# Kernel tuning notes

Measured on AMD Instinct MI355X. Metric: run time of the kernel, lower is better.

The kernel has to match this reference:

```python
import jax, jax.numpy as jnp
import numpy as np

N = 50000
E = 800000
IN_C, HID, LAT = 256, 128, 64


def setup_inputs() -> dict:
    key = jax.random.key(0)
    ks = jax.random.split(key, 8)
    x = jax.random.normal(ks[0], (N, IN_C), dtype=jnp.float32)
    edge_index = jax.random.randint(ks[1], (2, E), 0, N, dtype=jnp.int64)
    # Glorot-ish scaled weights (PyG GCNConv: Linear weight + separate bias)
    W1 = jax.random.normal(ks[2], (IN_C, HID), dtype=jnp.float32) / np.sqrt(IN_C)
    b1 = jnp.zeros((HID,), dtype=jnp.float32)
    Wmu = jax.random.normal(ks[3], (HID, LAT), dtype=jnp.float32) / np.sqrt(HID)
    bmu = jnp.zeros((LAT,), dtype=jnp.float32)
    Wlv = jax.random.normal(ks[4], (HID, LAT), dtype=jnp.float32) / np.sqrt(HID)
    blv = jnp.zeros((LAT,), dtype=jnp.float32)
    return {"x": x, "edge_index": edge_index, "W1": W1, "b1": b1,
            "Wmu": Wmu, "bmu": bmu, "Wlv": Wlv, "blv": blv}


def gcn_conv(x, edge_index, W, b):
    """PyG GCNConv: add self-loops, sym-normalize, transform, scatter-add."""
    n = x.shape[0]
    loop = jnp.arange(n, dtype=edge_index.dtype)
    row = jnp.concatenate([edge_index[0], loop])  # source
    col = jnp.concatenate([edge_index[1], loop])  # target
    deg = jax.ops.segment_sum(jnp.ones_like(col, dtype=x.dtype), col, num_segments=n)
    dinv = jax.lax.rsqrt(jnp.maximum(deg, 1e-12))  # deg >= 1 due to self-loops
    norm = dinv[row] * dinv[col]                   # [E+N]
    h = x @ W                                      # transform first (smaller width)
    msg = h[row] * norm[:, None]                   # [E+N, out] gathered messages
    out = jax.ops.segment_sum(msg, col, num_segments=n)
    return out + b


def reference(x, edge_index, W1, b1, Wmu, bmu, Wlv, blv):
    h = jax.nn.relu(gcn_conv(x, edge_index, W1, b1))
    # dropout p=0.0 -> identity
    mu = gcn_conv(h, edge_index, Wmu, bmu)
    logvar = gcn_conv(h, edge_index, Wlv, blv)
    return (mu, logvar)
```

## Files before the change

kernel.cpp:

```cpp
#include <hip/hip_runtime.h>
#include <stdint.h>

#define NN   50000
#define NE   800000
#define INC  256
#define HID  128
#define LAT  64

typedef unsigned short u16;
typedef short v8s __attribute__((ext_vector_type(8)));
typedef float v4f __attribute__((ext_vector_type(4)));

#define SLAB_OFF 0
#define OFFS_OFF 802816
#define W1P_OFF  881216
#define W2P_OFF  897600
#define G1_OFF   905792

#define NBIN        196
#define OFFS_STRIDE 200
#define NSLAB       784

#define G2_OFFU  8388608
#define C2_CNT   8388608
#define C2_DINV  8438608
#define C2_BKT   8488608

#define GB    782

__device__ __forceinline__ u16 f2b(float f) {
    union { float f; uint32_t i; } c; c.f = f;
    uint32_t r = c.i + 0x7FFF + ((c.i >> 16) & 1);
    return (u16)(r >> 16);
}
__device__ __forceinline__ float blo(unsigned u) { return __uint_as_float(u << 16); }
__device__ __forceinline__ float bhi(unsigned u) { return __uint_as_float(u & 0xffff0000u); }

__device__ void pack1_body(const float* __restrict__ W1, u16* __restrict__ W1P, int b) {
    int tg = b * 256 + threadIdx.x;
    int ks = tg >> 9, rem = tg & 511;
    int nt = rem >> 6, lane = rem & 63;
    int quad = lane >> 4, l15 = lane & 15;
    u16 o[8];
    #pragma unroll
    for (int j = 0; j < 8; j++)
        o[j] = f2b(W1[(long)(ks * 32 + quad * 8 + j) * HID + nt * 16 + l15]);
    *(ushort4*)(W1P + (long)tg * 8)     = make_ushort4(o[0], o[1], o[2], o[3]);
    *(ushort4*)(W1P + (long)tg * 8 + 4) = make_ushort4(o[4], o[5], o[6], o[7]);
}

__device__ void pack2_body(const float* __restrict__ Wmu, const float* __restrict__ Wlv,
                           u16* __restrict__ W2P, int b) {
    int tg = b * 256 + threadIdx.x;
    int ks = tg >> 9, rem = tg & 511;
    int nt = rem >> 6, lane = rem & 63;
    int quad = lane >> 4, l15 = lane & 15;
    const float* W = (nt < 4) ? Wmu : Wlv;
    int ntl = (nt < 4) ? nt : nt - 4;
    u16 o[8];
    #pragma unroll
    for (int j = 0; j < 8; j++)
        o[j] = f2b(W[(long)(ks * 32 + quad * 8 + j) * LAT + ntl * 16 + l15]);
    *(ushort4*)(W2P + (long)tg * 8)     = make_ushort4(o[0], o[1], o[2], o[3]);
    *(ushort4*)(W2P + (long)tg * 8 + 4) = make_ushort4(o[4], o[5], o[6], o[7]);
}

__global__ __launch_bounds__(256) void k_fusedA(unsigned* csr, const float* W1,
        const float* Wmu, const float* Wlv) {
    int b = blockIdx.x;
    if (b < 16) pack1_body(W1, (u16*)(csr + W1P_OFF), b);
    else pack2_body(Wmu, Wlv, (u16*)(csr + W2P_OFF), b - 16);
}

__device__ void gemm1_body(const float* __restrict__ xbuf,
        const unsigned* __restrict__ csr, u16* __restrict__ g1, int blk,
        u16* __restrict__ As) {
    const u16* W1P = (const u16*)(csr + W1P_OFF);
    int tid = threadIdx.x;
    int m0b = blk * 64;
    #pragma unroll
    for (int i = 0; i < 16; i++) {
        int idx = i * 256 + tid;
        int r = idx >> 6, c4 = idx & 63;
        int gr = m0b + r; gr = gr < NN ? gr : NN - 1;
        float4 a = *(const float4*)(xbuf + (long)gr * INC + c4 * 4);
        *(ushort4*)(As + r * 264 + c4 * 4) =
            make_ushort4(f2b(a.x), f2b(a.y), f2b(a.z), f2b(a.w));
    }
    __syncthreads();
    int lane = tid & 63, w = tid >> 6;
    int quad = lane >> 4, l15 = lane & 15;
    int m0 = m0b + w * 16;
    const v8s* bp = (const v8s*)W1P;
    v4f acc[8];
    #pragma unroll
    for (int t = 0; t < 8; t++) acc[t] = (v4f){0.f, 0.f, 0.f, 0.f};
    #pragma unroll
    for (int ks = 0; ks < 8; ks++) {
        v8s af = *(const v8s*)(As + (w * 16 + l15) * 264 + ks * 32 + quad * 8);
        #pragma unroll
        for (int t = 0; t < 8; t++) {
            v8s bf = bp[(ks * 8 + t) * 64 + lane];
            acc[t] = __builtin_amdgcn_mfma_f32_16x16x32_bf16(af, bf, acc[t], 0, 0, 0);
        }
    }
    #pragma unroll
    for (int r = 0; r < 4; r++) {
        int rr = m0 + quad * 4 + r;
        if (rr < NN) {
            u16* dst = g1 + (long)rr * HID + l15;
            #pragma unroll
            for (int t = 0; t < 8; t++) dst[t * 16] = f2b(acc[t][r]);
        }
    }
}

__device__ void part_body(const int* __restrict__ row, const int* __restrict__ col,
                          unsigned* __restrict__ csr, int id,
                          int* hist, int* scanbuf, unsigned* recs) {
    int tid = threadIdx.x;
    int base = id * 1024;
    hist[tid] = 0;
    __syncthreads();
    int v[4], u[4];
    #pragma unroll
    for (int i = 0; i < 4; i++) {
        int e = base + i * 256 + tid;
        if (e < NE) {
            v[i] = col[e]; u[i] = row[e];
            atomicAdd(&hist[v[i] >> 8], 1);
        } else v[i] = -1;
    }
    __syncthreads();
    int x = hist[tid];
    scanbuf[tid] = x;
    __syncthreads();
    for (int s = 1; s < 256; s <<= 1) {
        int y = (tid >= s) ? scanbuf[tid - s] : 0;
        __syncthreads();
        scanbuf[tid] += y;
        __syncthreads();
    }
    int excl = scanbuf[tid] - x;
    u16* offs = (u16*)(csr + OFFS_OFF) + (long)id * OFFS_STRIDE;
    if (tid <= NBIN) offs[tid] = (u16)excl;
    hist[tid] = excl;
    __syncthreads();
    #pragma unroll
    for (int i = 0; i < 4; i++) {
        if (v[i] >= 0) {
            int slot = atomicAdd(&hist[v[i] >> 8], 1);
            recs[slot] = (unsigned)u[i] | ((unsigned)(v[i] & 255) << 16);
        }
    }
    __syncthreads();
    unsigned* slab = csr + SLAB_OFF + (long)id * 1024;
    #pragma unroll
    for (int i = 0; i < 4; i++) slab[i * 256 + tid] = recs[i * 256 + tid];
}

__global__ __launch_bounds__(256) void k_fusedB(const float* __restrict__ xbuf,
        unsigned* __restrict__ csr, u16* __restrict__ g1,
        const int* __restrict__ row, const int* __restrict__ col) {
    __shared__ __align__(16) u16 As[64 * 264];
    __shared__ int hist[256];
    __shared__ int scanbuf[256];
    __shared__ unsigned recs[1024];
    int b = blockIdx.x;
    if (b < GB) gemm1_body(xbuf, csr, g1, b, As);
    part_body(row, col, csr, b, hist, scanbuf, recs);
}

__global__ __launch_bounds__(256) void k_merge(const unsigned* __restrict__ csr,
        unsigned* __restrict__ xb) {
    __shared__ int cnt_lds[256];
    __shared__ u16 bkt_lds[256 * 64];
    int tid = threadIdx.x;
    int bin = blockIdx.x;
    cnt_lds[tid] = 0;
    __syncthreads();
    const u16* offs = (const u16*)(csr + OFFS_OFF);
    const unsigned* slab = csr + SLAB_OFF;
    for (int s = tid; s < NSLAB; s += 256) {
        int st = offs[s * OFFS_STRIDE + bin];
        int en = offs[s * OFFS_STRIDE + bin + 1];
        for (int j = st; j < en; j++) {
            unsigned r = slab[s * 1024 + j];
            int vlo = (int)(r >> 16);
            int slot = atomicAdd(&cnt_lds[vlo], 1);
            if (slot < 64) bkt_lds[(vlo << 6) + slot] = (u16)(r & 0xffffu);
        }
    }
    __syncthreads();
    int* cnt2 = (int*)(xb + C2_CNT);
    float* dinv = (float*)(xb + C2_DINV);
    u16* bkt2 = (u16*)(xb + C2_BKT);
    int v0 = bin << 8;
    {
        int v = v0 + tid;
        if (v < NN) {
            int deg = cnt_lds[tid];
            int cn = deg < 64 ? deg : 64;
            cnt2[v] = cn;
            dinv[v] = rsqrtf((float)(deg + 1));
        }
    }
    const uint4* src = (const uint4*)bkt_lds;
    #pragma unroll
    for (int i = 0; i < 8; i++) {
        int idx = i * 256 + tid;
        int node = idx >> 3;
        if (v0 + node < NN)
            ((uint4*)(bkt2 + ((long)(v0 + node) << 6)))[idx & 7] = src[idx];
    }
}

#define EACC(D, W) { \
    a0 += D * blo(W.x); a1 += D * bhi(W.x); a2 += D * blo(W.y); a3 += D * bhi(W.y); \
    a4 += D * blo(W.z); a5 += D * bhi(W.z); a6 += D * blo(W.w); a7 += D * bhi(W.w); }

#define GATHER_NODE(SRC) \
    float a0, a1, a2, a3, a4, a5, a6, a7; \
    { uint4 wv = *(const uint4*)(SRC + (long)vc * HID + lane16 * 8); \
      a0 = dvv * blo(wv.x); a1 = dvv * bhi(wv.x); a2 = dvv * blo(wv.y); a3 = dvv * bhi(wv.y); \
      a4 = dvv * blo(wv.z); a5 = dvv * bhi(wv.z); a6 = dvv * blo(wv.w); a7 = dvv * bhi(wv.w); } \
    { const u16* bk = bkt2 + ((long)vc << 6); \
      int e = 0; \
      for (; e + 3 < cn; e += 4) { \
          ushort4 ii = *(const ushort4*)(bk + e); \
          float d0 = dinv[ii.x], d1 = dinv[ii.y], d2 = dinv[ii.z], d3 = dinv[ii.w]; \
          uint4 w0 = *(const uint4*)(SRC + (long)ii.x * HID + lane16 * 8); \
          uint4 w1 = *(const uint4*)(SRC + (long)ii.y * HID + lane16 * 8); \
          uint4 w2 = *(const uint4*)(SRC + (long)ii.z * HID + lane16 * 8); \
          uint4 w3 = *(const uint4*)(SRC + (long)ii.w * HID + lane16 * 8); \
          EACC(d0, w0) EACC(d1, w1) EACC(d2, w2) EACC(d3, w3) \
      } \
      for (; e < cn; e++) { \
          int i0 = bk[e]; \
          float d0 = dinv[i0]; \
          uint4 w0 = *(const uint4*)(SRC + (long)i0 * HID + lane16 * 8); \
          EACC(d0, w0) \
      } }

#define HPAD 136
__global__ __launch_bounds__(512, 4) void k_fusedD(const u16* __restrict__ g1,
        const unsigned* __restrict__ xb, const float* __restrict__ b1,
        const unsigned* __restrict__ csr, u16* __restrict__ g2) {
    __shared__ __align__(16) u16 hs[64 * HPAD];
    int tid = threadIdx.x;
    int lane16 = tid & 15, grp = tid >> 4;
    const int* cnt2 = (const int*)(xb + C2_CNT);
    const float* dinv = (const float*)(xb + C2_DINV);
    const u16* bkt2 = (const u16*)(xb + C2_BKT);
    int m0b = blockIdx.x * 64;

    #pragma unroll 1
    for (int pass = 0; pass < 2; pass++) {
        int nl = pass * 32 + grp;
        int v = m0b + nl;
        int vc = v < NN ? v : NN - 1;
        int cn = cnt2[vc];
        float dvv = dinv[vc];
        GATHER_NODE(g1)
        int j = lane16 * 8;
        float r[8] = {a0, a1, a2, a3, a4, a5, a6, a7};
        unsigned p[4];
        #pragma unroll
        for (int i = 0; i < 4; i++) {
            float x0 = dvv * r[2 * i]     + b1[j + 2 * i];
            float x1 = dvv * r[2 * i + 1] + b1[j + 2 * i + 1];
            x0 = x0 > 0.f ? x0 : 0.f;
            x1 = x1 > 0.f ? x1 : 0.f;
            p[i] = (unsigned)f2b(x0) | ((unsigned)f2b(x1) << 16);
        }
        *(uint4*)(hs + nl * HPAD + j) = make_uint4(p[0], p[1], p[2], p[3]);
    }
    __syncthreads();

    if (tid < 256) {
        const u16* W2P = (const u16*)(csr + W2P_OFF);
        int lane = tid & 63, w = tid >> 6;
        int quad = lane >> 4, l15 = lane & 15;
        int m0 = m0b + w * 16;
        const v8s* bp = (const v8s*)W2P;
        v4f acc[8];
        #pragma unroll
        for (int t = 0; t < 8; t++) acc[t] = (v4f){0.f, 0.f, 0.f, 0.f};
        #pragma unroll
        for (int ks = 0; ks < 4; ks++) {
            v8s af = *(const v8s*)(hs + (w * 16 + l15) * HPAD + ks * 32 + quad * 8);
            #pragma unroll
            for (int t = 0; t < 8; t++) {
                v8s bf = bp[(ks * 8 + t) * 64 + lane];
                acc[t] = __builtin_amdgcn_mfma_f32_16x16x32_bf16(af, bf, acc[t], 0, 0, 0);
            }
        }
        #pragma unroll
        for (int r = 0; r < 4; r++) {
            int rr = m0 + quad * 4 + r;
            if (rr < NN) {
                u16* dst = g2 + (long)rr * HID + l15;
                #pragma unroll
                for (int t = 0; t < 8; t++) dst[t * 16] = f2b(acc[t][r]);
            }
        }
    }
}

__global__ __launch_bounds__(256) void k_gather2(const u16* __restrict__ g2,
        const unsigned* __restrict__ xb, const float* __restrict__ bmu,
        const float* __restrict__ blv, float* __restrict__ out) {
    int tid = threadIdx.x;
    int lane16 = tid & 15, grp = tid >> 4;
    int vc = blockIdx.x * 16 + grp;
    const int* cnt2 = (const int*)(xb + C2_CNT);
    const float* dinv = (const float*)(xb + C2_DINV);
    const u16* bkt2 = (const u16*)(xb + C2_BKT);
    int cn = cnt2[vc];
    float dvv = dinv[vc];
    GATHER_NODE(g2)
    float r[8] = {a0, a1, a2, a3, a4, a5, a6, a7};
    if (lane16 < 8) {
        int j = lane16 * 8;
        float4 o0 = make_float4(dvv * r[0] + bmu[j],     dvv * r[1] + bmu[j + 1],
                                dvv * r[2] + bmu[j + 2], dvv * r[3] + bmu[j + 3]);
        float4 o1 = make_float4(dvv * r[4] + bmu[j + 4], dvv * r[5] + bmu[j + 5],
                                dvv * r[6] + bmu[j + 6], dvv * r[7] + bmu[j + 7]);
        float* dst = out + (long)vc * LAT + j;
        *(float4*)dst = o0;
        *(float4*)(dst + 4) = o1;
    } else {
        int j = lane16 * 8 - 64;
        float4 o0 = make_float4(dvv * r[0] + blv[j],     dvv * r[1] + blv[j + 1],
                                dvv * r[2] + blv[j + 2], dvv * r[3] + blv[j + 3]);
        float4 o1 = make_float4(dvv * r[4] + blv[j + 4], dvv * r[5] + blv[j + 5],
                                dvv * r[6] + blv[j + 6], dvv * r[7] + blv[j + 7]);
        float* dst = out + (long)NN * LAT + (long)vc * LAT + j;
        *(float4*)dst = o0;
        *(float4*)(dst + 4) = o1;
    }
}

extern "C" void kernel_launch(void* const* d_in, const int* in_sizes, int n_in,
                              void* d_out, int out_size, void* d_ws, size_t ws_size,
                              hipStream_t stream) {
    float* xbuf = (float*)d_in[0];
    const int* ei  = (const int*)d_in[1];
    const float* W1  = (const float*)d_in[2];
    const float* b1  = (const float*)d_in[3];
    const float* Wmu = (const float*)d_in[4];
    const float* bmu = (const float*)d_in[5];
    const float* Wlv = (const float*)d_in[6];
    const float* blv = (const float*)d_in[7];
    const int* row = ei;
    const int* col = ei + NE;

    unsigned* csr = (unsigned*)d_out;
    u16* g1   = (u16*)(csr + G1_OFF);
    u16* g2   = (u16*)xbuf + G2_OFFU;
    unsigned* xb = (unsigned*)xbuf;

    k_fusedA<<<24, 256, 0, stream>>>(csr, W1, Wmu, Wlv);

    k_fusedB<<<NSLAB, 256, 0, stream>>>(xbuf, csr, g1, row, col);
    k_merge <<<NBIN, 256, 0, stream>>>(csr, xb);

    k_fusedD<<<GB, 512, 0, stream>>>(g1, xb, b1, csr, g2);

    k_gather2<<<NN / 16, 256, 0, stream>>>(g2, xb, bmu, blv, (float*)d_out);
}
```

Baseline: 209.5 us.

## Slice feature matrices into 16-column planes and split gather from second GEMM

After: 265.4 us. 26.7% more time.

```diff
diff --git a/kernel.cpp b/kernel.cpp
--- a/kernel.cpp
+++ b/kernel.cpp
@@ -27,6 +27,7 @@
 #define C2_BKT   8488608
 
 #define GB    782
+#define SGB   12504
 
 __device__ __forceinline__ u16 f2b(float f) {
     union { float f; uint32_t i; } c; c.f = f;
@@ -108,9 +109,9 @@
     for (int r = 0; r < 4; r++) {
         int rr = m0 + quad * 4 + r;
         if (rr < NN) {
-            u16* dst = g1 + (long)rr * HID + l15;
             #pragma unroll
-            for (int t = 0; t < 8; t++) dst[t * 16] = f2b(acc[t][r]);
+            for (int t = 0; t < 8; t++)
+                g1[((long)t * NN + rr) * 16 + l15] = f2b(acc[t][r]);
         }
     }
 }
@@ -215,129 +216,139 @@
     }
 }
 
-#define EACC(D, W) { \
-    a0 += D * blo(W.x); a1 += D * bhi(W.x); a2 += D * blo(W.y); a3 += D * bhi(W.y); \
-    a4 += D * blo(W.z); a5 += D * bhi(W.z); a6 += D * blo(W.w); a7 += D * bhi(W.w); }
-
-#define GATHER_NODE(SRC) \
-    float a0, a1, a2, a3, a4, a5, a6, a7; \
-    { uint4 wv = *(const uint4*)(SRC + (long)vc * HID + lane16 * 8); \
-      a0 = dvv * blo(wv.x); a1 = dvv * bhi(wv.x); a2 = dvv * blo(wv.y); a3 = dvv * bhi(wv.y); \
-      a4 = dvv * blo(wv.z); a5 = dvv * bhi(wv.z); a6 = dvv * blo(wv.w); a7 = dvv * bhi(wv.w); } \
+#define SEACC(D, W) { a0 += D * blo(W); a1 += D * bhi(W); }
+#define SGATHER(SRC) \
+    float a0, a1; \
+    { unsigned wv = *(const unsigned*)(SRC + (long)vc * 16 + co); \
+      a0 = dvv * blo(wv); a1 = dvv * bhi(wv); } \
     { const u16* bk = bkt2 + ((long)vc << 6); \
       int e = 0; \
+      for (; e + 7 < cn; e += 8) { \
+          ushort4 iA = *(const ushort4*)(bk + e); \
+          ushort4 iB = *(const ushort4*)(bk + e + 4); \
+          float d0 = dinv[iA.x], d1 = dinv[iA.y], d2 = dinv[iA.z], d3 = dinv[iA.w]; \
+          float d4 = dinv[iB.x], d5 = dinv[iB.y], d6 = dinv[iB.z], d7 = dinv[iB.w]; \
+          unsigned w0 = *(const unsigned*)(SRC + (long)iA.x * 16 + co); \
+          unsigned w1 = *(const unsigned*)(SRC + (long)iA.y * 16 + co); \
+          unsigned w2 = *(const unsigned*)(SRC + (long)iA.z * 16 + co); \
+          unsigned w3 = *(const unsigned*)(SRC + (long)iA.w * 16 + co); \
+          unsigned w4 = *(const unsigned*)(SRC + (long)iB.x * 16 + co); \
+          unsigned w5 = *(const unsigned*)(SRC + (long)iB.y * 16 + co); \
+          unsigned w6 = *(const unsigned*)(SRC + (long)iB.z * 16 + co); \
+          unsigned w7 = *(const unsigned*)(SRC + (long)iB.w * 16 + co); \
+          SEACC(d0, w0) SEACC(d1, w1) SEACC(d2, w2) SEACC(d3, w3) \
+          SEACC(d4, w4) SEACC(d5, w5) SEACC(d6, w6) SEACC(d7, w7) \
+      } \
       for (; e + 3 < cn; e += 4) { \
           ushort4 ii = *(const ushort4*)(bk + e); \
           float d0 = dinv[ii.x], d1 = dinv[ii.y], d2 = dinv[ii.z], d3 = dinv[ii.w]; \
-          uint4 w0 = *(const uint4*)(SRC + (long)ii.x * HID + lane16 * 8); \
-          uint4 w1 = *(const uint4*)(SRC + (long)ii.y * HID + lane16 * 8); \
-          uint4 w2 = *(const uint4*)(SRC + (long)ii.z * HID + lane16 * 8); \
-          uint4 w3 = *(const uint4*)(SRC + (long)ii.w * HID + lane16 * 8); \
-          EACC(d0, w0) EACC(d1, w1) EACC(d2, w2) EACC(d3, w3) \
+          unsigned w0 = *(const unsigned*)(SRC + (long)ii.x * 16 + co); \
+          unsigned w1 = *(const unsigned*)(SRC + (long)ii.y * 16 + co); \
+          unsigned w2 = *(const unsigned*)(SRC + (long)ii.z * 16 + co); \
+          unsigned w3 = *(const unsigned*)(SRC + (long)ii.w * 16 + co); \
+          SEACC(d0, w0) SEACC(d1, w1) SEACC(d2, w2) SEACC(d3, w3) \
       } \
       for (; e < cn; e++) { \
           int i0 = bk[e]; \
           float d0 = dinv[i0]; \
-          uint4 w0 = *(const uint4*)(SRC + (long)i0 * HID + lane16 * 8); \
-          EACC(d0, w0) \
+          unsigned w0 = *(const unsigned*)(SRC + (long)i0 * 16 + co); \
+          SEACC(d0, w0) \
       } }
 
-#define HPAD 136
-__global__ __launch_bounds__(512, 4) void k_fusedD(const u16* __restrict__ g1,
+__global__ __launch_bounds__(256) void k_gath1(const u16* __restrict__ g1s,
         const unsigned* __restrict__ xb, const float* __restrict__ b1,
-        const unsigned* __restrict__ csr, u16* __restrict__ g2) {
-    __shared__ __align__(16) u16 hs[64 * HPAD];
-    int tid = threadIdx.x;
-    int lane16 = tid & 15, grp = tid >> 4;
-    const int* cnt2 = (const int*)(xb + C2_CNT);
-    const float* dinv = (const float*)(xb + C2_DINV);
-    const u16* bkt2 = (const u16*)(xb + C2_BKT);
-    int m0b = blockIdx.x * 64;
-
-    #pragma unroll 1
-    for (int pass = 0; pass < 2; pass++) {
-        int nl = pass * 32 + grp;
-        int v = m0b + nl;
-        int vc = v < NN ? v : NN - 1;
-        int cn = cnt2[vc];
-        float dvv = dinv[vc];
-        GATHER_NODE(g1)
-        int j = lane16 * 8;
-        float r[8] = {a0, a1, a2, a3, a4, a5, a6, a7};
-        unsigned p[4];
-        #pragma unroll
-        for (int i = 0; i < 4; i++) {
-            float x0 = dvv * r[2 * i]     + b1[j + 2 * i];
-            float x1 = dvv * r[2 * i + 1] + b1[j + 2 * i + 1];
-            x0 = x0 > 0.f ? x0 : 0.f;
-            x1 = x1 > 0.f ? x1 : 0.f;
-            p[i] = (unsigned)f2b(x0) | ((unsigned)f2b(x1) << 16);
-        }
-        *(uint4*)(hs + nl * HPAD + j) = make_uint4(p[0], p[1], p[2], p[3]);
-    }
-    __syncthreads();
-
-    if (tid < 256) {
-        const u16* W2P = (const u16*)(csr + W2P_OFF);
-        int lane = tid & 63, w = tid >> 6;
-        int quad = lane >> 4, l15 = lane & 15;
-        int m0 = m0b + w * 16;
-        const v8s* bp = (const v8s*)W2P;
-        v4f acc[8];
-        #pragma unroll
-        for (int t = 0; t < 8; t++) acc[t] = (v4f){0.f, 0.f, 0.f, 0.f};
-        #pragma unroll
-        for (int ks = 0; ks < 4; ks++) {
-            v8s af = *(const v8s*)(hs + (w * 16 + l15) * HPAD + ks * 32 + quad * 8);
-            #pragma unroll
-            for (int t = 0; t < 8; t++) {
-                v8s bf = bp[(ks * 8 + t) * 64 + lane];
-                acc[t] = __builtin_amdgcn_mfma_f32_16x16x32_bf16(af, bf, acc[t], 0, 0, 0);
-            }
-        }
-        #pragma unroll
-        for (int r = 0; r < 4; r++) {
-            int rr = m0 + quad * 4 + r;
-            if (rr < NN) {
-                u16* dst = g2 + (long)rr * HID + l15;
-                #pragma unroll
-                for (int t = 0; t < 8; t++) dst[t * 16] = f2b(acc[t][r]);
-            }
-        }
-    }
-}
-
-__global__ __launch_bounds__(256) void k_gather2(const u16* __restrict__ g2,
-        const unsigned* __restrict__ xb, const float* __restrict__ bmu,
-        const float* __restrict__ blv, float* __restrict__ out) {
-    int tid = threadIdx.x;
-    int lane16 = tid & 15, grp = tid >> 4;
-    int vc = blockIdx.x * 16 + grp;
+        u16* __restrict__ hs) {
+    int tid = threadIdx.x;
+    int l8 = tid & 7, grp = tid >> 3;
+    int s = blockIdx.x & 7;
+    int tile = blockIdx.x >> 3;
+    int v = tile * 32 + grp;
+    int vc = v < NN ? v : NN - 1;
     const int* cnt2 = (const int*)(xb + C2_CNT);
     const float* dinv = (const float*)(xb + C2_DINV);
     const u16* bkt2 = (const u16*)(xb + C2_BKT);
     int cn = cnt2[vc];
     float dvv = dinv[vc];
-    GATHER_NODE(g2)
-    float r[8] = {a0, a1, a2, a3, a4, a5, a6, a7};
-    if (lane16 < 8) {
-        int j = lane16 * 8;
-        float4 o0 = make_float4(dvv * r[0] + bmu[j],     dvv * r[1] + bmu[j + 1],
-                                dvv * r[2] + bmu[j + 2], dvv * r[3] + bmu[j + 3]);
-        float4 o1 = make_float4(dvv * r[4] + bmu[j + 4], dvv * r[5] + bmu[j + 5],
-                                dvv * r[6] + bmu[j + 6], dvv * r[7] + bmu[j + 7]);
-        float* dst = out + (long)vc * LAT + j;
-        *(float4*)dst = o0;
-        *(float4*)(dst + 4) = o1;
-    } else {
-        int j = lane16 * 8 - 64;
-        float4 o0 = make_float4(dvv * r[0] + blv[j],     dvv * r[1] + blv[j + 1],
-                                dvv * r[2] + blv[j + 2], dvv * r[3] + blv[j + 3]);
-        float4 o1 = make_float4(dvv * r[4] + blv[j + 4], dvv * r[5] + blv[j + 5],
-                                dvv * r[6] + blv[j + 6], dvv * r[7] + blv[j + 7]);
-        float* dst = out + (long)NN * LAT + (long)vc * LAT + j;
-        *(float4*)dst = o0;
-        *(float4*)(dst + 4) = o1;
+    const u16* gsl = g1s + (long)s * NN * 16;
+    int co = l8 * 2;
+    SGATHER(gsl)
+    if (v < NN) {
+        int j = s * 16 + co;
+        float x0 = dvv * a0 + b1[j];
+        float x1 = dvv * a1 + b1[j + 1];
+        x0 = x0 > 0.f ? x0 : 0.f;
+        x1 = x1 > 0.f ? x1 : 0.f;
+        *(unsigned*)(hs + ((long)s * NN + v) * 16 + co) =
+            (unsigned)f2b(x0) | ((unsigned)f2b(x1) << 16);
+    }
+}
+
+__global__ __launch_bounds__(256) void k_gemm2(const u16* __restrict__ hs,
+        const unsigned* __restrict__ csr, u16* __restrict__ g2s) {
+    const u16* W2P = (const u16*)(csr + W2P_OFF);
+    int tid = threadIdx.x;
+    int lane = tid & 63, w = tid >> 6;
+    int quad = lane >> 4, l15 = lane & 15;
+    int m0 = blockIdx.x * 64 + w * 16;
+    int arow = m0 + l15;
+    int arc = arow < NN ? arow : NN - 1;
+    const v8s* bp = (const v8s*)W2P;
+    v4f acc[8];
+    #pragma unroll
+    for (int t = 0; t < 8; t++) acc[t] = (v4f){0.f, 0.f, 0.f, 0.f};
+
+    v8s af[4];
+    #pragma unroll
+    for (int ks = 0; ks < 4; ks++) {
+        int colb = ks * 32 + quad * 8;
+        af[ks] = *(const v8s*)(hs + ((long)(colb >> 4) * NN + arc) * 16 + (colb & 15));
+    }
+    #pragma unroll
+    for (int ks = 0; ks < 4; ks++) {
+        #pragma unroll
+        for (int t = 0; t < 8; t++) {
+            v8s bf = bp[(ks * 8 + t) * 64 + lane];
+            acc[t] = __builtin_amdgcn_mfma_f32_16x16x32_bf16(af[ks], bf, acc[t], 0, 0, 0);
+        }
+    }
+    #pragma unroll
+    for (int r = 0; r < 4; r++) {
+        int rr = m0 + quad * 4 + r;
+        if (rr < NN) {
+            #pragma unroll
+            for (int t = 0; t < 8; t++)
+                g2s[((long)t * NN + rr) * 16 + l15] = f2b(acc[t][r]);
+        }
+    }
+}
+
+__global__ __launch_bounds__(256) void k_gath2(const u16* __restrict__ g2s,
+        const unsigned* __restrict__ xb, const float* __restrict__ bmu,
+        const float* __restrict__ blv, float* __restrict__ out) {
+    int tid = threadIdx.x;
+    int l8 = tid & 7, grp = tid >> 3;
+    int s = blockIdx.x & 7;
+    int tile = blockIdx.x >> 3;
+    int v = tile * 32 + grp;
+    int vc = v < NN ? v : NN - 1;
+    const int* cnt2 = (const int*)(xb + C2_CNT);
+    const float* dinv = (const float*)(xb + C2_DINV);
+    const u16* bkt2 = (const u16*)(xb + C2_BKT);
+    int cn = cnt2[vc];
+    float dvv = dinv[vc];
+    const u16* gsl = g2s + (long)s * NN * 16;
+    int co = l8 * 2;
+    SGATHER(gsl)
+    if (v < NN) {
+        int j = s * 16 + co;
+        if (j < 64) {
+            *(float2*)(out + (long)v * LAT + j) =
+                make_float2(dvv * a0 + bmu[j], dvv * a1 + bmu[j + 1]);
+        } else {
+            int jl = j - 64;
+            *(float2*)(out + (long)NN * LAT + (long)v * LAT + jl) =
+                make_float2(dvv * a0 + blv[jl], dvv * a1 + blv[jl + 1]);
+        }
     }
 }
 
@@ -356,16 +367,17 @@
     const int* col = ei + NE;
 
     unsigned* csr = (unsigned*)d_out;
-    u16* g1   = (u16*)(csr + G1_OFF);
-    u16* g2   = (u16*)xbuf + G2_OFFU;
+    u16* g1s  = (u16*)(csr + G1_OFF);
+    u16* hs   = (u16*)xbuf;
+    u16* g2s  = (u16*)xbuf + G2_OFFU;
     unsigned* xb = (unsigned*)xbuf;
 
     k_fusedA<<<24, 256, 0, stream>>>(csr, W1, Wmu, Wlv);
 
-    k_fusedB<<<NSLAB, 256, 0, stream>>>(xbuf, csr, g1, row, col);
+    k_fusedB<<<NSLAB, 256, 0, stream>>>(xbuf, csr, g1s, row, col);
     k_merge <<<NBIN, 256, 0, stream>>>(csr, xb);
 
-    k_fusedD<<<GB, 512, 0, stream>>>(g1, xb, b1, csr, g2);
-
-    k_gather2<<<NN / 16, 256, 0, stream>>>(g2, xb, bmu, blv, (float*)d_out);
-}
+    k_gath1<<<SGB, 256, 0, stream>>>(g1s, xb, b1, hs);
+    k_gemm2<<<GB, 256, 0, stream>>>(hs, csr, g2s);
+    k_gath2<<<SGB, 256, 0, stream>>>(g2s, xb, bmu, blv, (float*)d_out);
+}
```
